# Performance work log

Measured on AMD Instinct MI355X. Metric: run time of the kernel, lower is better.

The kernel has to match this reference:

```python
import jax, jax.numpy as jnp
import numpy as np

N, E = 20000, 320000
DIMS = [(200, 64), (64, 128), (128, 256), (256, 256), (256, 512)]


def _embed(v):
    # NeRF positional encoding, multires=10, include_input, log-sampled freqs, [sin, cos] per freq
    freqs = 2.0 ** jnp.arange(10, dtype=jnp.float32)
    ang = v[:, None, :] * freqs[None, :, None]           # [N, 10, 3]
    sc = jnp.stack([jnp.sin(ang), jnp.cos(ang)], 2)      # [N, 10, 2, 3] (freq-major, sin then cos)
    return jnp.concatenate([v, sc.reshape(v.shape[0], -1)], -1)  # [N, 63]


def _edge_conv(h, src, dst, w1, b1, w2, b2):
    # PyG EdgeConv: nn([x_i, x_j - x_i]) aggregated by mean onto target i
    hi = h[dst]
    hj = h[src]
    m = jnp.concatenate([hi, hj - hi], -1)               # [E, 2*in]
    m = jax.nn.relu(m @ w1 + b1) @ w2 + b2               # [E, out]
    s = jax.ops.segment_sum(m, dst, num_segments=N)
    cnt = jax.ops.segment_sum(jnp.ones((m.shape[0], 1), m.dtype), dst, num_segments=N)
    return s / jnp.maximum(cnt, 1.0)                     # scatter-mean (0 for isolated nodes)


def _bn(h, g, b):
    # training-mode BatchNorm1d over nodes (biased variance, eps=1e-5)
    mu = h.mean(0)
    var = ((h - mu) ** 2).mean(0)
    return g * (h - mu) * jax.lax.rsqrt(var + 1e-5) + b


def setup_inputs() -> dict:
    key = jax.random.key(0)
    keys = iter(jax.random.split(key, 64))
    inp = {
        "x": jax.random.normal(next(keys), (N, 20), jnp.float32),
        "edge_index": jax.random.randint(next(keys), (2, E), 0, N, jnp.int32),
        "batch": jnp.zeros((N,), jnp.int32),
    }
    for i, (din, dout) in enumerate(DIMS, 1):
        inp[f"gc{i}_w1"] = jax.random.normal(next(keys), (2 * din, dout), jnp.float32) / np.sqrt(2.0 * din)
        inp[f"gc{i}_b1"] = jnp.zeros((dout,), jnp.float32)
        inp[f"gc{i}_w2"] = jax.random.normal(next(keys), (dout, dout), jnp.float32) / np.sqrt(1.0 * dout)
        inp[f"gc{i}_b2"] = jnp.zeros((dout,), jnp.float32)
    for i, d in enumerate([64, 128, 256, 256], 1):
        inp[f"n{i}_g"] = jnp.ones((d,), jnp.float32)
        inp[f"n{i}_b"] = jnp.zeros((d,), jnp.float32)
    return inp


def reference(x, edge_index, batch,
              gc1_w1, gc1_b1, gc1_w2, gc1_b2,
              gc2_w1, gc2_b1, gc2_w2, gc2_b2,
              gc3_w1, gc3_b1, gc3_w2, gc3_b2,
              gc4_w1, gc4_b1, gc4_w2, gc4_b2,
              gc5_w1, gc5_b1, gc5_w2, gc5_b2,
              n1_g, n1_b, n2_g, n2_b, n3_g, n3_b, n4_g, n4_b):
    src, dst = edge_index[0], edge_index[1]
    h = jnp.concatenate(
        [_embed(x[:, 0:3]), _embed(x[:, 3:6]), _embed(x[:, 6:9]), x[:, 9:20]], -1)  # [N, 200]
    h = jax.nn.relu(_bn(_edge_conv(h, src, dst, gc1_w1, gc1_b1, gc1_w2, gc1_b2), n1_g, n1_b))
    h = jax.nn.relu(_bn(_edge_conv(h, src, dst, gc2_w1, gc2_b1, gc2_w2, gc2_b2), n2_g, n2_b))
    h = jax.nn.relu(_bn(_edge_conv(h, src, dst, gc3_w1, gc3_b1, gc3_w2, gc3_b2), n3_g, n3_b))
    h = jax.nn.relu(_bn(_edge_conv(h, src, dst, gc4_w1, gc4_b1, gc4_w2, gc4_b2), n4_g, n4_b))
    return _edge_conv(h, src, dst, gc5_w1, gc5_b1, gc5_w2, gc5_b2)  # [N, 512]
```

## Files before the change

kernel.cpp:

```cpp
#include <hip/hip_runtime.h>
#include <math.h>

#define NNODES 20000
#define NEDGES 320000
#define NB 79
#define MBLK 157
#define MQ 19
#define MR 5

typedef __bf16 bf16x8 __attribute__((ext_vector_type(8)));
typedef float f32x4 __attribute__((ext_vector_type(4)));
typedef unsigned short u16x8 __attribute__((ext_vector_type(8)));

__device__ inline unsigned short f2bf(float x) {
  union { float f; unsigned int u; } q;
  q.f = x;
  unsigned int u = q.u;
  unsigned int r = (u + 0x7fffu + ((u >> 16) & 1u)) >> 16;
  return (unsigned short)r;
}

__device__ inline float bf2f(unsigned short u) {
  union { unsigned int u; float f; } q;
  q.u = ((unsigned int)u) << 16;
  return q.f;
}

__device__ inline void load_lds16(const unsigned short* g, unsigned short* l) {
  __builtin_amdgcn_global_load_lds(
      (const __attribute__((address_space(1))) unsigned int*)g,
      (__attribute__((address_space(3))) unsigned int*)l, 16, 0, 0);
}

__global__ __launch_bounds__(256) void init_kernel(int* __restrict__ cnt,
                                                   float* __restrict__ stats) {
  int idx = blockIdx.x * 256 + threadIdx.x;
  if (idx < NNODES) cnt[idx] = 0;
  int j = idx - NNODES;
  if (j >= 0 && j < 4096) stats[j] = 0.f;
}

__global__ __launch_bounds__(256) void count_embed_kernel(
    const int* __restrict__ edst, int* __restrict__ cnt,
    const float* __restrict__ x, unsigned short* __restrict__ h) {
  int bid = blockIdx.x;
  if (bid < 1250) {
    int e = bid * 256 + threadIdx.x;
    atomicAdd(&cnt[edst[e]], 1);
    return;
  }
  int n = (bid - 1250) * 256 + threadIdx.x;
  if (n >= NNODES) return;
  const float* xr = x + (size_t)n * 20;
  unsigned short* hr = h + (size_t)n * 256;
#pragma unroll
  for (int g = 0; g < 3; ++g) {
    float v0 = xr[g * 3 + 0], v1 = xr[g * 3 + 1], v2 = xr[g * 3 + 2];
    unsigned short* o = hr + g * 63;
    o[0] = f2bf(v0); o[1] = f2bf(v1); o[2] = f2bf(v2);
    float f = 1.0f;
    for (int fr = 0; fr < 10; ++fr) {
      float s0, c0, s1, c1, s2, c2;
      sincosf(v0 * f, &s0, &c0);
      sincosf(v1 * f, &s1, &c1);
      sincosf(v2 * f, &s2, &c2);
      int base = 3 + fr * 6;
      o[base + 0] = f2bf(s0); o[base + 1] = f2bf(s1); o[base + 2] = f2bf(s2);
      o[base + 3] = f2bf(c0); o[base + 4] = f2bf(c1); o[base + 5] = f2bf(c2);
      f *= 2.0f;
    }
  }
  for (int j = 0; j < 11; ++j) hr[189 + j] = f2bf(xr[9 + j]);
  for (int j = 200; j < 256; ++j) hr[j] = 0;
}

__global__ __launch_bounds__(256) void scan_pass1(const int* __restrict__ cnt,
                                                  int* __restrict__ bsum) {
  __shared__ int red[256];
  int i = blockIdx.x * 256 + threadIdx.x;
  int v = (i < NNODES) ? cnt[i] : 0;
  red[threadIdx.x] = v;
  __syncthreads();
#pragma unroll
  for (int off = 128; off > 0; off >>= 1) {
    if (threadIdx.x < off) red[threadIdx.x] += red[threadIdx.x + off];
    __syncthreads();
  }
  if (threadIdx.x == 0) bsum[blockIdx.x] = red[0];
}

__global__ __launch_bounds__(128) void scan_pass2(const int* __restrict__ bsum,
                                                  int* __restrict__ boff) {
  __shared__ int buf[128];
  int t = threadIdx.x;
  int v = (t < NB) ? bsum[t] : 0;
  buf[t] = v;
  __syncthreads();
#pragma unroll
  for (int off = 1; off < 128; off <<= 1) {
    int u = (t >= off) ? buf[t - off] : 0;
    __syncthreads();
    buf[t] += u;
    __syncthreads();
  }
  if (t < NB) boff[t] = buf[t] - v;
}

__global__ __launch_bounds__(256) void scan_pass3(const int* __restrict__ cnt,
                                                  const int* __restrict__ boff,
                                                  int* __restrict__ rowptr,
                                                  int* __restrict__ head) {
  __shared__ int buf[256];
  int i = blockIdx.x * 256 + threadIdx.x;
  int v = (i < NNODES) ? cnt[i] : 0;
  buf[threadIdx.x] = v;
  __syncthreads();
#pragma unroll
  for (int off = 1; off < 256; off <<= 1) {
    int u = (threadIdx.x >= off) ? buf[threadIdx.x - off] : 0;
    __syncthreads();
    buf[threadIdx.x] += u;
    __syncthreads();
  }
  if (i < NNODES) {
    int excl = boff[blockIdx.x] + buf[threadIdx.x] - v;
    rowptr[i] = excl;
    head[i] = excl;
  }
  if (i == 0) rowptr[NNODES] = NEDGES;
}

struct WPtrs {
  const float* w1[5];
  const float* w2[5];
};

#define WT1_TOTAL 507904
#define WT2_TOTAL 413696

__global__ __launch_bounds__(256) void scatter_prep_kernel(
    const int* __restrict__ esrc, const int* __restrict__ edst,
    int* __restrict__ head, int* __restrict__ csr_src, WPtrs p,
    unsigned short* __restrict__ Wt1All, unsigned short* __restrict__ Wt2All) {
  int bid = blockIdx.x;
  if (bid < 1250) {
    int e = bid * 256 + threadIdx.x;
    int pos = atomicAdd(&head[edst[e]], 1);
    csr_src[pos] = esrc[e];
    return;
  }
  int idx = (bid - 1250) * 256 + threadIdx.x;
  if (idx < WT1_TOTAL) {
    int L, off, din, dout, Kpad;
    if (idx < 32768)       { L = 0; off = 0;      din = 200; dout = 64;  Kpad = 256; }
    else if (idx < 49152)  { L = 1; off = 32768;  din = 64;  dout = 128; Kpad = 64;  }
    else if (idx < 114688) { L = 2; off = 49152;  din = 128; dout = 256; Kpad = 128; }
    else if (idx < 245760) { L = 3; off = 114688; din = 256; dout = 256; Kpad = 256; }
    else                   { L = 4; off = 245760; din = 256; dout = 512; Kpad = 256; }
    int local = idx - off;
    int c = local / Kpad, k = local % Kpad;
    float v = 0.f;
    if (k < din)
      v = (c < dout) ? p.w1[L][(size_t)k * dout + c]
                     : p.w1[L][(size_t)(din + k) * dout + (c - dout)];
    Wt1All[idx] = f2bf(v);
    return;
  }
  int jdx = idx - WT1_TOTAL;
  if (jdx >= WT2_TOTAL) return;
  int L, off, d;
  if (jdx < 4096)        { L = 0; off = 0;      d = 64;  }
  else if (jdx < 20480)  { L = 1; off = 4096;   d = 128; }
  else if (jdx < 86016)  { L = 2; off = 20480;  d = 256; }
  else if (jdx < 151552) { L = 3; off = 86016;  d = 256; }
  else                   { L = 4; off = 151552; d = 512; }
  int local = jdx - off;
  int n = local / d, k = local % d;
  Wt2All[jdx] = f2bf(p.w2[L][(size_t)k * d + n]);
}

template <int EPI, int EPIA>
__global__ __launch_bounds__(256) void gemm128_kernel(
    const void* __restrict__ Aptr, int lda, int K, int ncolb,
    const unsigned short* __restrict__ Bt, int Ncol, int dhalf,
    const float* __restrict__ bias, const int* __restrict__ cnt,
    const float* __restrict__ pstats, const float* __restrict__ pg,
    const float* __restrict__ pb, float* __restrict__ stats,
    void* __restrict__ Cout) {
  int bid = blockIdx.x;
  int xcd = bid & 7;
  int j = bid >> 3;
  int cntx = MQ + (xcd < MR ? 1 : 0);
  int row_local = j / ncolb;
  if (row_local >= cntx) return;
  int colb = j - row_local * ncolb;
  int row0 = xcd * MQ + min(xcd, MR);
  int bR = (row0 + row_local) * 128;
  int bC = colb * 128;

  __shared__ unsigned short sA[128 * 64];
  __shared__ unsigned short sB[128 * 64];
  __shared__ float sScale[256], sShift[256];
  int tid = threadIdx.x;
  int wid = tid >> 6, lane = tid & 63;
  int wr = wid >> 1, wc = wid & 1;
  int lr = lane & 15, lg = lane >> 4;
  int sub = lane >> 3;
  int ckl = (lane & 7) ^ sub;

  if (EPIA == 1) {
    for (int c = tid; c < K; c += 256) {
      float mu = pstats[c] * (1.0f / NNODES);
      float var = pstats[K + c] * (1.0f / NNODES) - mu * mu;
      float sc = pg[c] * rsqrtf(var + 1e-5f);
      sScale[c] = sc;
      sShift[c] = pb[c] - mu * sc;
    }
    __syncthreads();
  }

  f32x4 acc[4][4];
#pragma unroll
  for (int fr = 0; fr < 4; ++fr)
#pragma unroll
    for (int fc = 0; fc < 4; ++fc) acc[fr][fc] = f32x4{0.f, 0.f, 0.f, 0.f};

  for (int k0 = 0; k0 < K; k0 += 64) {
    if (EPIA == 0) {
      const unsigned short* Ab = (const unsigned short*)Aptr;
#pragma unroll
      for (int q = 0; q < 4; ++q) {
        int t = wid * 4 + q;
        int gr = bR + t * 8 + sub;
        if (gr > NNODES - 1) gr = NNODES - 1;
        load_lds16(Ab + (size_t)gr * lda + k0 + ckl * 8, sA + t * 512);
      }
    } else {
      const float* Af = (const float*)Aptr;
#pragma unroll
      for (int i = 0; i < 4; ++i) {
        int idx = tid + i * 256;
        int row = idx >> 3, c = idx & 7;
        int gr = bR + row;
        u16x8 o;
        if (gr < NNODES) {
          float4 u0 = *(const float4*)(Af + (size_t)gr * lda + k0 + c * 8);
          float4 u1 = *(const float4*)(Af + (size_t)gr * lda + k0 + c * 8 + 4);
          float uv[8] = {u0.x, u0.y, u0.z, u0.w, u1.x, u1.y, u1.z, u1.w};
#pragma unroll
          for (int jj = 0; jj < 8; ++jj) {
            int k = k0 + c * 8 + jj;
            o[jj] = f2bf(fmaxf(uv[jj] * sScale[k] + sShift[k], 0.f));
          }
        } else {
#pragma unroll
          for (int jj = 0; jj < 8; ++jj) o[jj] = 0;
        }
        int ck = c ^ (row & 7);
        *(u16x8*)(sA + row * 64 + ck * 8) = o;
      }
    }
#pragma unroll
    for (int q = 0; q < 4; ++q) {
      int t = wid * 4 + q;
      int gn = bC + t * 8 + sub;
      load_lds16(Bt + (size_t)gn * K + k0 + ckl * 8, sB + t * 512);
    }
    __syncthreads();
#pragma unroll
    for (int ks = 0; ks < 2; ++ks) {
      bf16x8 aF[4], bF[4];
      int cb = ks * 4 + lg;
      int ck = cb ^ (lr & 7);
#pragma unroll
      for (int fr = 0; fr < 4; ++fr)
        aF[fr] = *(const bf16x8*)(sA + (wr * 64 + fr * 16 + lr) * 64 + ck * 8);
#pragma unroll
      for (int fc = 0; fc < 4; ++fc)
        bF[fc] = *(const bf16x8*)(sB + (wc * 64 + fc * 16 + lr) * 64 + ck * 8);
#pragma unroll
      for (int fr = 0; fr < 4; ++fr)
#pragma unroll
        for (int fc = 0; fc < 4; ++fc)
          acc[fr][fc] = __builtin_amdgcn_mfma_f32_16x16x32_bf16(
              aF[fr], bF[fc], acc[fr][fc], 0, 0, 0);
    }
    __syncthreads();
  }

  float csum[4] = {0.f, 0.f, 0.f, 0.f}, csum2[4] = {0.f, 0.f, 0.f, 0.f};
#pragma unroll
  for (int fr = 0; fr < 4; ++fr) {
#pragma unroll
    for (int jj = 0; jj < 4; ++jj) {
      int gr = bR + wr * 64 + fr * 16 + lg * 4 + jj;
      if (gr >= NNODES) continue;
      int ct = (EPI >= 1) ? cnt[gr] : 1;
#pragma unroll
      for (int fc = 0; fc < 4; ++fc) {
        int gc = bC + wc * 64 + fc * 16 + lr;
        float v = acc[fr][fc][jj];
        if (EPI == 0) {
          if (gc < dhalf) v += bias[gc];
          ((unsigned short*)Cout)[(size_t)gr * Ncol + gc] = f2bf(v);
        } else {
          v = (ct > 0) ? (v + bias[gc]) : 0.f;
          ((float*)Cout)[(size_t)gr * Ncol + gc] = v;
          if (EPI == 2) {
            csum[fc] += v;
            csum2[fc] += v * v;
          }
        }
      }
    }
  }
  if (EPI == 2) {
#pragma unroll
    for (int fc = 0; fc < 4; ++fc) {
      float s = csum[fc], s2 = csum2[fc];
      s += __shfl_xor(s, 16, 64);
      s += __shfl_xor(s, 32, 64);
      s2 += __shfl_xor(s2, 16, 64);
      s2 += __shfl_xor(s2, 32, 64);
      if (lg == 0) {
        int gc = bC + wc * 64 + fc * 16 + lr;
        atomicAdd(&stats[gc], s);
        atomicAdd(&stats[Ncol + gc], s2);
      }
    }
  }
}

__global__ __launch_bounds__(256) void gemm64_stats_kernel(
    const unsigned short* __restrict__ A, int lda, int K,
    const unsigned short* __restrict__ Bt, int Ncol,
    const float* __restrict__ bias, const int* __restrict__ cnt,
    float* __restrict__ stats, float* __restrict__ Cout) {
  __shared__ unsigned short sA[128 * 40];
  __shared__ unsigned short sB[64 * 40];
  int tid = threadIdx.x;
  int bR = blockIdx.y * 128, bC = blockIdx.x * 64;
  int wid = tid >> 6, lane = tid & 63;
  int wr = wid >> 1, wc = wid & 1;
  int lr = lane & 15, lg = lane >> 4;

  f32x4 acc[4][2];
#pragma unroll
  for (int fr = 0; fr < 4; ++fr)
#pragma unroll
    for (int fc = 0; fc < 2; ++fc) acc[fr][fc] = f32x4{0.f, 0.f, 0.f, 0.f};

  for (int k0 = 0; k0 < K; k0 += 32) {
#pragma unroll
    for (int rep = 0; rep < 2; ++rep) {
      int idx = tid + rep * 256;
      int row = idx >> 2, kq = (idx & 3) * 8;
      int gr = bR + row;
      bf16x8 v;
      if (gr < NNODES) {
        v = *(const bf16x8*)(A + (size_t)gr * lda + k0 + kq);
      } else {
#pragma unroll
        for (int i = 0; i < 8; ++i) v[i] = (__bf16)0.f;
      }
      *(bf16x8*)(sA + row * 40 + kq) = v;
    }
    {
      int n = tid >> 2, kq = (tid & 3) * 8;
      bf16x8 v = *(const bf16x8*)(Bt + (size_t)(bC + n) * K + k0 + kq);
      *(bf16x8*)(sB + n * 40 + kq) = v;
    }
    __syncthreads();
    bf16x8 aF[4], bF[2];
#pragma unroll
    for (int fr = 0; fr < 4; ++fr)
      aF[fr] = *(const bf16x8*)(sA + (wr * 64 + fr * 16 + lr) * 40 + lg * 8);
#pragma unroll
    for (int fc = 0; fc < 2; ++fc)
      bF[fc] = *(const bf16x8*)(sB + (wc * 32 + fc * 16 + lr) * 40 + lg * 8);
#pragma unroll
    for (int fr = 0; fr < 4; ++fr)
#pragma unroll
      for (int fc = 0; fc < 2; ++fc)
        acc[fr][fc] = __builtin_amdgcn_mfma_f32_16x16x32_bf16(
            aF[fr], bF[fc], acc[fr][fc], 0, 0, 0);
    __syncthreads();
  }

  float csum[2] = {0.f, 0.f}, csum2[2] = {0.f, 0.f};
#pragma unroll
  for (int fr = 0; fr < 4; ++fr) {
#pragma unroll
    for (int j = 0; j < 4; ++j) {
      int gr = bR + wr * 64 + fr * 16 + lg * 4 + j;
      if (gr >= NNODES) continue;
      int ct = cnt[gr];
#pragma unroll
      for (int fc = 0; fc < 2; ++fc) {
        int gc = bC + wc * 32 + fc * 16 + lr;
        float v = acc[fr][fc][j];
        v = (ct > 0) ? (v + bias[gc]) : 0.f;
        Cout[(size_t)gr * Ncol + gc] = v;
        csum[fc] += v;
        csum2[fc] += v * v;
      }
    }
  }
#pragma unroll
  for (int fc = 0; fc < 2; ++fc) {
    float s = csum[fc], s2 = csum2[fc];
    s += __shfl_xor(s, 16, 64);
    s += __shfl_xor(s, 32, 64);
    s2 += __shfl_xor(s2, 16, 64);
    s2 += __shfl_xor(s2, 32, 64);
    if (lg == 0) {
      int gc = bC + wc * 32 + fc * 16 + lr;
      atomicAdd(&stats[gc], s);
      atomicAdd(&stats[Ncol + gc], s2);
    }
  }
}

template <int D, int SLICES>
__global__ __launch_bounds__(256) void edge_agg_kernel(
    const unsigned short* __restrict__ AV, const int* __restrict__ rowptr,
    const int* __restrict__ csr_src, unsigned short* __restrict__ Y) {
  int slice = blockIdx.x % SLICES;
  int ngrp = blockIdx.x / SLICES;
  int tid = threadIdx.x;
  int ln = tid & 7;
  int sn = tid >> 3;
  int node = ngrp * 32 + sn;
  if (node >= NNODES) return;
  int c = slice * 64 + ln * 8;
  const unsigned short* Arow = AV + (size_t)node * 2 * D;
  u16x8 a8 = *(const u16x8*)(Arow + c);
  u16x8 v8 = *(const u16x8*)(Arow + D + c);
  float ad[8], acc[8];
#pragma unroll
  for (int i = 0; i < 8; ++i) {
    ad[i] = bf2f(a8[i]) - bf2f(v8[i]);
    acc[i] = 0.f;
  }
  int e0 = rowptr[node], e1 = rowptr[node + 1];
  int e = e0;
  for (; e + 3 < e1; e += 4) {
    int s0 = csr_src[e], s1 = csr_src[e + 1];
    int s2 = csr_src[e + 2], s3 = csr_src[e + 3];
    u16x8 w0 = *(const u16x8*)(AV + (size_t)s0 * 2 * D + D + c);
    u16x8 w1 = *(const u16x8*)(AV + (size_t)s1 * 2 * D + D + c);
    u16x8 w2 = *(const u16x8*)(AV + (size_t)s2 * 2 * D + D + c);
    u16x8 w3 = *(const u16x8*)(AV + (size_t)s3 * 2 * D + D + c);
#pragma unroll
    for (int i = 0; i < 8; ++i) {
      acc[i] += fmaxf(ad[i] + bf2f(w0[i]), 0.f) + fmaxf(ad[i] + bf2f(w1[i]), 0.f) +
                fmaxf(ad[i] + bf2f(w2[i]), 0.f) + fmaxf(ad[i] + bf2f(w3[i]), 0.f);
    }
  }
  for (; e < e1; ++e) {
    int s0 = csr_src[e];
    u16x8 w0 = *(const u16x8*)(AV + (size_t)s0 * 2 * D + D + c);
#pragma unroll
    for (int i = 0; i < 8; ++i) acc[i] += fmaxf(ad[i] + bf2f(w0[i]), 0.f);
  }
  float inv = (e1 > e0) ? 1.f / (float)(e1 - e0) : 0.f;
  u16x8 o;
#pragma unroll
  for (int i = 0; i < 8; ++i) o[i] = f2bf(acc[i] * inv);
  *(u16x8*)(Y + (size_t)node * D + c) = o;
}

static void launch_edge_agg(int dout, const unsigned short* AV, const int* rowptr,
                            const int* csr_src, unsigned short* Y,
                            hipStream_t st) {
  const int NG = (NNODES + 31) / 32;
  switch (dout) {
    case 64:
      hipLaunchKernelGGL((edge_agg_kernel<64, 1>), dim3(NG * 1), dim3(256), 0, st,
                         AV, rowptr, csr_src, Y);
      break;
    case 128:
      hipLaunchKernelGGL((edge_agg_kernel<128, 2>), dim3(NG * 2), dim3(256), 0, st,
                         AV, rowptr, csr_src, Y);
      break;
    case 256:
      hipLaunchKernelGGL((edge_agg_kernel<256, 4>), dim3(NG * 4), dim3(256), 0, st,
                         AV, rowptr, csr_src, Y);
      break;
    case 512:
      hipLaunchKernelGGL((edge_agg_kernel<512, 8>), dim3(NG * 8), dim3(256), 0, st,
                         AV, rowptr, csr_src, Y);
      break;
  }
}

extern "C" void kernel_launch(void* const* d_in, const int* in_sizes, int n_in,
                              void* d_out, int out_size, void* d_ws,
                              size_t ws_size, hipStream_t stream) {
  const float* x = (const float*)d_in[0];
  const int* edge_index = (const int*)d_in[1];
  const int* esrc = edge_index;
  const int* edst = edge_index + NEDGES;

  const float* gw1[5] = {(const float*)d_in[3],  (const float*)d_in[7],
                         (const float*)d_in[11], (const float*)d_in[15],
                         (const float*)d_in[19]};
  const float* gb1[5] = {(const float*)d_in[4],  (const float*)d_in[8],
                         (const float*)d_in[12], (const float*)d_in[16],
                         (const float*)d_in[20]};
  const float* gw2[5] = {(const float*)d_in[5],  (const float*)d_in[9],
                         (const float*)d_in[13], (const float*)d_in[17],
                         (const float*)d_in[21]};
  const float* gb2[5] = {(const float*)d_in[6],  (const float*)d_in[10],
                         (const float*)d_in[14], (const float*)d_in[18],
                         (const float*)d_in[22]};
  const float* ng[4] = {(const float*)d_in[23], (const float*)d_in[25],
                        (const float*)d_in[27], (const float*)d_in[29]};
  const float* nb[4] = {(const float*)d_in[24], (const float*)d_in[26],
                        (const float*)d_in[28], (const float*)d_in[30]};

  unsigned short* AV = (unsigned short*)d_ws;
  float* S = (float*)(AV + (size_t)NNODES * 1024);
  unsigned short* Hbf = (unsigned short*)(S + (size_t)NNODES * 256);
  unsigned short* Ybf = Hbf + (size_t)NNODES * 256;
  unsigned short* Wt1All = Ybf + (size_t)NNODES * 512;
  unsigned short* Wt2All = Wt1All + WT1_TOTAL;
  int* cnt = (int*)(Wt2All + WT2_TOTAL);
  int* rowptr = cnt + NNODES;
  int* head = rowptr + NNODES + 1;
  int* csr_src = head + NNODES;
  int* bsum = csr_src + NEDGES;
  int* boff = bsum + NB;
  float* stats = (float*)(boff + NB);

  const int Kpads[5] = {256, 64, 128, 256, 256};
  const int douts[5] = {64, 128, 256, 256, 512};
  const int wt1_off[5] = {0, 32768, 49152, 114688, 245760};
  const int wt2_off[5] = {0, 4096, 20480, 86016, 151552};

  WPtrs wp;
  for (int i = 0; i < 5; ++i) { wp.w1[i] = gw1[i]; wp.w2[i] = gw2[i]; }

  init_kernel<<<(NNODES + 4096 + 255) / 256, 256, 0, stream>>>(cnt, stats);
  count_embed_kernel<<<1250 + NB, 256, 0, stream>>>(edst, cnt, x, Hbf);
  scan_pass1<<<NB, 256, 0, stream>>>(cnt, bsum);
  scan_pass2<<<1, 128, 0, stream>>>(bsum, boff);
  scan_pass3<<<NB, 256, 0, stream>>>(cnt, boff, rowptr, head);
  scatter_prep_kernel<<<1250 + (WT1_TOTAL + WT2_TOTAL + 255) / 256, 256, 0, stream>>>(
      esrc, edst, head, csr_src, wp, Wt1All, Wt2All);

  int lda = 256;
  for (int L = 0; L < 5; ++L) {
    int Kp = Kpads[L], dout = douts[L];
    {
      int ncolb = 2 * dout / 128;
      if (ncolb < 1) ncolb = 1;
      dim3 g1(8 * (MQ + 1) * ncolb);
      if (L == 0) {
        hipLaunchKernelGGL((gemm128_kernel<0, 0>), g1, dim3(256), 0, stream,
                           (const void*)Hbf, lda, Kp, ncolb, Wt1All + wt1_off[L],
                           2 * dout, dout, gb1[L], (const int*)nullptr,
                           (const float*)nullptr, (const float*)nullptr,
                           (const float*)nullptr, (float*)nullptr, (void*)AV);
      } else {
        hipLaunchKernelGGL((gemm128_kernel<0, 1>), g1, dim3(256), 0, stream,
                           (const void*)S, Kp, Kp, ncolb, Wt1All + wt1_off[L],
                           2 * dout, dout, gb1[L], (const int*)nullptr,
                           stats + (L - 1) * 1024, ng[L - 1], nb[L - 1],
                           (float*)nullptr, (void*)AV);
      }
    }
    launch_edge_agg(dout, AV, rowptr, csr_src, Ybf, stream);
    if (L == 0) {
      dim3 g2(1, MBLK);
      gemm64_stats_kernel<<<g2, 256, 0, stream>>>(
          Ybf, dout, dout, Wt2All + wt2_off[L], dout, gb2[L], cnt,
          stats + L * 1024, S);
    } else if (L < 4) {
      int ncolb = dout / 128;
      dim3 g2(8 * (MQ + 1) * ncolb);
      hipLaunchKernelGGL((gemm128_kernel<2, 0>), g2, dim3(256), 0, stream,
                         (const void*)Ybf, dout, dout, ncolb, Wt2All + wt2_off[L],
                         dout, dout, gb2[L], cnt, (const float*)nullptr,
                         (const float*)nullptr, (const float*)nullptr,
                         stats + L * 1024, (void*)S);
    } else {
      int ncolb = dout / 128;
      dim3 g2(8 * (MQ + 1) * ncolb);
      hipLaunchKernelGGL((gemm128_kernel<1, 0>), g2, dim3(256), 0, stream,
                         (const void*)Ybf, dout, dout, ncolb, Wt2All + wt2_off[L],
                         dout, dout, gb2[L], cnt, (const float*)nullptr,
                         (const float*)nullptr, (const float*)nullptr,
                         (float*)nullptr, (void*)d_out);
    }
  }
}
```

Measured before the change: 448.1 us.

## Double-buffer LDS tiles in node GEMM to overlap global loads with MFMA

Turns the node-level GEMM's K loop into a two-stage pipeline: A and B tiles for the next K step are fetched into a second LDS buffer while MFMAs run on the current one, with one barrier per iteration instead of two. For the BN-fused input path, the fp32 prefetch goes into registers and the BN+ReLU+bf16 conversion is written to the next buffer after the MFMAs. BN scale/shift is now computed per thread from stats rather than through a shared-memory table. This doubles LDS use, which may reduce occupancy, and adds register pressure from the prefetched floats.

After: 482.0 us. +7.6%, slower.

```diff
diff --git a/kernel.cpp b/kernel.cpp
--- a/kernel.cpp
+++ b/kernel.cpp
@@ -177,6 +177,44 @@
   int local = jdx - off;
   int n = local / d, k = local % d;
   Wt2All[jdx] = f2bf(p.w2[L][(size_t)k * d + n]);
+}
+
+__device__ inline void bn_convert_store(const float4* pre, const float* pstats,
+                                        const float* pg, const float* pb, int K,
+                                        int kb, int tid, unsigned short* dst) {
+  float4 m0 = *(const float4*)(pstats + kb);
+  float4 m1 = *(const float4*)(pstats + kb + 4);
+  float4 q0 = *(const float4*)(pstats + K + kb);
+  float4 q1 = *(const float4*)(pstats + K + kb + 4);
+  float4 g0 = *(const float4*)(pg + kb);
+  float4 g1 = *(const float4*)(pg + kb + 4);
+  float4 b0 = *(const float4*)(pb + kb);
+  float4 b1 = *(const float4*)(pb + kb + 4);
+  float mu8[8] = {m0.x, m0.y, m0.z, m0.w, m1.x, m1.y, m1.z, m1.w};
+  float q8[8] = {q0.x, q0.y, q0.z, q0.w, q1.x, q1.y, q1.z, q1.w};
+  float g8[8] = {g0.x, g0.y, g0.z, g0.w, g1.x, g1.y, g1.z, g1.w};
+  float b8[8] = {b0.x, b0.y, b0.z, b0.w, b1.x, b1.y, b1.z, b1.w};
+  float sc[8], sh[8];
+#pragma unroll
+  for (int j = 0; j < 8; ++j) {
+    float mu = mu8[j] * (1.0f / NNODES);
+    float var = q8[j] * (1.0f / NNODES) - mu * mu;
+    float s = g8[j] * rsqrtf(var + 1e-5f);
+    sc[j] = s;
+    sh[j] = b8[j] - mu * s;
+  }
+#pragma unroll
+  for (int i = 0; i < 4; ++i) {
+    int idx = tid + i * 256;
+    int row = idx >> 3;
+    int ck = (tid & 7) ^ (row & 7);
+    const float* u = (const float*)&pre[i * 2];
+    u16x8 o;
+#pragma unroll
+    for (int j = 0; j < 8; ++j)
+      o[j] = f2bf(fmaxf(u[j] * sc[j] + sh[j], 0.f));
+    *(u16x8*)(dst + row * 64 + ck * 8) = o;
+  }
 }
 
 template <int EPI, int EPIA>
@@ -198,9 +236,8 @@
   int bR = (row0 + row_local) * 128;
   int bC = colb * 128;
 
-  __shared__ unsigned short sA[128 * 64];
-  __shared__ unsigned short sB[128 * 64];
-  __shared__ float sScale[256], sShift[256];
+  __shared__ unsigned short sA0[128 * 64], sA1[128 * 64];
+  __shared__ unsigned short sB0[128 * 64], sB1[128 * 64];
   int tid = threadIdx.x;
   int wid = tid >> 6, lane = tid & 63;
   int wr = wid >> 1, wc = wid & 1;
@@ -208,65 +245,91 @@
   int sub = lane >> 3;
   int ckl = (lane & 7) ^ sub;
 
-  if (EPIA == 1) {
-    for (int c = tid; c < K; c += 256) {
-      float mu = pstats[c] * (1.0f / NNODES);
-      float var = pstats[K + c] * (1.0f / NNODES) - mu * mu;
-      float sc = pg[c] * rsqrtf(var + 1e-5f);
-      sScale[c] = sc;
-      sShift[c] = pb[c] - mu * sc;
-    }
-    __syncthreads();
-  }
-
   f32x4 acc[4][4];
 #pragma unroll
   for (int fr = 0; fr < 4; ++fr)
 #pragma unroll
     for (int fc = 0; fc < 4; ++fc) acc[fr][fc] = f32x4{0.f, 0.f, 0.f, 0.f};
 
-  for (int k0 = 0; k0 < K; k0 += 64) {
-    if (EPIA == 0) {
-      const unsigned short* Ab = (const unsigned short*)Aptr;
+  unsigned short* cA = sA0;
+  unsigned short* cB = sB0;
+  unsigned short* nA = sA1;
+  unsigned short* nB = sB1;
+  const int nt = K >> 6;
+
+  if (EPIA == 0) {
+    const unsigned short* Ab = (const unsigned short*)Aptr;
+#pragma unroll
+    for (int q = 0; q < 4; ++q) {
+      int tt = wid * 4 + q;
+      int gr = bR + tt * 8 + sub;
+      if (gr > NNODES - 1) gr = NNODES - 1;
+      load_lds16(Ab + (size_t)gr * lda + ckl * 8, cA + tt * 512);
+    }
+  } else {
+    const float* Af = (const float*)Aptr;
+    float4 pre[8];
+#pragma unroll
+    for (int i = 0; i < 4; ++i) {
+      int idx = tid + i * 256;
+      int gr = bR + (idx >> 3);
+      if (gr < NNODES) {
+        pre[i * 2] = *(const float4*)(Af + (size_t)gr * lda + (tid & 7) * 8);
+        pre[i * 2 + 1] = *(const float4*)(Af + (size_t)gr * lda + (tid & 7) * 8 + 4);
+      } else {
+        pre[i * 2] = float4{0.f, 0.f, 0.f, 0.f};
+        pre[i * 2 + 1] = float4{0.f, 0.f, 0.f, 0.f};
+      }
+    }
+    bn_convert_store(pre, pstats, pg, pb, K, (tid & 7) * 8, tid, cA);
+  }
+#pragma unroll
+  for (int q = 0; q < 4; ++q) {
+    int tt = wid * 4 + q;
+    int gn = bC + tt * 8 + sub;
+    load_lds16(Bt + (size_t)gn * K + ckl * 8, cB + tt * 512);
+  }
+  __syncthreads();
+
+  for (int t = 0; t < nt; ++t) {
+    __builtin_amdgcn_sched_barrier(0);
+    const bool pf = (t + 1 < nt);
+    const int k1 = (t + 1) << 6;
+    float4 pre[8];
+    if (pf) {
+      if (EPIA == 0) {
+        const unsigned short* Ab = (const unsigned short*)Aptr;
+#pragma unroll
+        for (int q = 0; q < 4; ++q) {
+          int tt = wid * 4 + q;
+          int gr = bR + tt * 8 + sub;
+          if (gr > NNODES - 1) gr = NNODES - 1;
+          load_lds16(Ab + (size_t)gr * lda + k1 + ckl * 8, nA + tt * 512);
+        }
+      } else {
+        const float* Af = (const float*)Aptr;
+#pragma unroll
+        for (int i = 0; i < 4; ++i) {
+          int idx = tid + i * 256;
+          int gr = bR + (idx >> 3);
+          if (gr < NNODES) {
+            pre[i * 2] = *(const float4*)(Af + (size_t)gr * lda + k1 + (tid & 7) * 8);
+            pre[i * 2 + 1] =
+                *(const float4*)(Af + (size_t)gr * lda + k1 + (tid & 7) * 8 + 4);
+          } else {
+            pre[i * 2] = float4{0.f, 0.f, 0.f, 0.f};
+            pre[i * 2 + 1] = float4{0.f, 0.f, 0.f, 0.f};
+          }
+        }
+      }
 #pragma unroll
       for (int q = 0; q < 4; ++q) {
-        int t = wid * 4 + q;
-        int gr = bR + t * 8 + sub;
-        if (gr > NNODES - 1) gr = NNODES - 1;
-        load_lds16(Ab + (size_t)gr * lda + k0 + ckl * 8, sA + t * 512);
-      }
-    } else {
-      const float* Af = (const float*)Aptr;
-#pragma unroll
-      for (int i = 0; i < 4; ++i) {
-        int idx = tid + i * 256;
-        int row = idx >> 3, c = idx & 7;
-        int gr = bR + row;
-        u16x8 o;
-        if (gr < NNODES) {
-          float4 u0 = *(const float4*)(Af + (size_t)gr * lda + k0 + c * 8);
-          float4 u1 = *(const float4*)(Af + (size_t)gr * lda + k0 + c * 8 + 4);
-          float uv[8] = {u0.x, u0.y, u0.z, u0.w, u1.x, u1.y, u1.z, u1.w};
-#pragma unroll
-          for (int jj = 0; jj < 8; ++jj) {
-            int k = k0 + c * 8 + jj;
-            o[jj] = f2bf(fmaxf(uv[jj] * sScale[k] + sShift[k], 0.f));
-          }
-        } else {
-#pragma unroll
-          for (int jj = 0; jj < 8; ++jj) o[jj] = 0;
-        }
-        int ck = c ^ (row & 7);
-        *(u16x8*)(sA + row * 64 + ck * 8) = o;
-      }
-    }
-#pragma unroll
-    for (int q = 0; q < 4; ++q) {
-      int t = wid * 4 + q;
-      int gn = bC + t * 8 + sub;
-      load_lds16(Bt + (size_t)gn * K + k0 + ckl * 8, sB + t * 512);
-    }
-    __syncthreads();
+        int tt = wid * 4 + q;
+        int gn = bC + tt * 8 + sub;
+        load_lds16(Bt + (size_t)gn * K + k1 + ckl * 8, nB + tt * 512);
+      }
+    }
+    __builtin_amdgcn_sched_barrier(0);
 #pragma unroll
     for (int ks = 0; ks < 2; ++ks) {
       bf16x8 aF[4], bF[4];
@@ -274,10 +337,10 @@
       int ck = cb ^ (lr & 7);
 #pragma unroll
       for (int fr = 0; fr < 4; ++fr)
-        aF[fr] = *(const bf16x8*)(sA + (wr * 64 + fr * 16 + lr) * 64 + ck * 8);
+        aF[fr] = *(const bf16x8*)(cA + (wr * 64 + fr * 16 + lr) * 64 + ck * 8);
 #pragma unroll
       for (int fc = 0; fc < 4; ++fc)
-        bF[fc] = *(const bf16x8*)(sB + (wc * 64 + fc * 16 + lr) * 64 + ck * 8);
+        bF[fc] = *(const bf16x8*)(cB + (wc * 64 + fc * 16 + lr) * 64 + ck * 8);
 #pragma unroll
       for (int fr = 0; fr < 4; ++fr)
 #pragma unroll
@@ -285,7 +348,14 @@
           acc[fr][fc] = __builtin_amdgcn_mfma_f32_16x16x32_bf16(
               aF[fr], bF[fc], acc[fr][fc], 0, 0, 0);
     }
-    __syncthreads();
+    __builtin_amdgcn_sched_barrier(0);
+    if (EPIA == 1 && pf)
+      bn_convert_store(pre, pstats, pg, pb, K, k1 + (tid & 7) * 8, tid, nA);
+    asm volatile("s_waitcnt vmcnt(0) lgkmcnt(0)" ::: "memory");
+    __builtin_amdgcn_s_barrier();
+    unsigned short* tp;
+    tp = cA; cA = nA; nA = tp;
+    tp = cB; cB = nB; nB = tp;
   }
 
   float csum[4] = {0.f, 0.f, 0.f, 0.f}, csum2[4] = {0.f, 0.f, 0.f, 0.f};
```

## Store pre-BatchNorm layer outputs in bf16 and fold block-offset scan into pass3

Applied to the files above, without the earlier changes.

The second GEMM's output S, which is the pre-BatchNorm activation, is now written as bf16 instead of fp32. The next layer's A-load reads it as bf16 and applies the BN scale, shift and ReLU after converting back, which halves the store and reload traffic for that intermediate. Statistics are still accumulated in fp32 before rounding. Separately, the single-block scan_pass2 launch is removed and every pass3 block recomputes the 79-entry prefix itself, trading redundant work for one fewer launch. The bf16 rounding of the pre-BN values adds some precision loss.

Result: no change. 447.7 us (-0.1%).

```diff
diff --git a/kernel.cpp b/kernel.cpp
--- a/kernel.cpp
+++ b/kernel.cpp
@@ -89,41 +89,39 @@
   if (threadIdx.x == 0) bsum[blockIdx.x] = red[0];
 }
 
-__global__ __launch_bounds__(128) void scan_pass2(const int* __restrict__ bsum,
-                                                  int* __restrict__ boff) {
-  __shared__ int buf[128];
+__global__ __launch_bounds__(256) void scan_pass3(const int* __restrict__ cnt,
+                                                  const int* __restrict__ bsum,
+                                                  int* __restrict__ rowptr,
+                                                  int* __restrict__ head) {
+  __shared__ int pref[128];
+  __shared__ int buf[256];
   int t = threadIdx.x;
-  int v = (t < NB) ? bsum[t] : 0;
+  if (t < 128) {
+    int v = (t < NB) ? bsum[t] : 0;
+    pref[t] = v;
+  }
+  __syncthreads();
+#pragma unroll
+  for (int off = 1; off < 128; off <<= 1) {
+    int u = (t < 128 && t >= off) ? pref[t - off] : 0;
+    __syncthreads();
+    if (t < 128) pref[t] += u;
+    __syncthreads();
+  }
+  int boff = (blockIdx.x == 0) ? 0 : pref[blockIdx.x - 1];
+  int i = blockIdx.x * 256 + t;
+  int v = (i < NNODES) ? cnt[i] : 0;
   buf[t] = v;
   __syncthreads();
 #pragma unroll
-  for (int off = 1; off < 128; off <<= 1) {
+  for (int off = 1; off < 256; off <<= 1) {
     int u = (t >= off) ? buf[t - off] : 0;
     __syncthreads();
     buf[t] += u;
     __syncthreads();
   }
-  if (t < NB) boff[t] = buf[t] - v;
-}
-
-__global__ __launch_bounds__(256) void scan_pass3(const int* __restrict__ cnt,
-                                                  const int* __restrict__ boff,
-                                                  int* __restrict__ rowptr,
-                                                  int* __restrict__ head) {
-  __shared__ int buf[256];
-  int i = blockIdx.x * 256 + threadIdx.x;
-  int v = (i < NNODES) ? cnt[i] : 0;
-  buf[threadIdx.x] = v;
-  __syncthreads();
-#pragma unroll
-  for (int off = 1; off < 256; off <<= 1) {
-    int u = (threadIdx.x >= off) ? buf[threadIdx.x - off] : 0;
-    __syncthreads();
-    buf[threadIdx.x] += u;
-    __syncthreads();
-  }
   if (i < NNODES) {
-    int excl = boff[blockIdx.x] + buf[threadIdx.x] - v;
+    int excl = boff + buf[t] - v;
     rowptr[i] = excl;
     head[i] = excl;
   }
@@ -236,7 +234,7 @@
         load_lds16(Ab + (size_t)gr * lda + k0 + ckl * 8, sA + t * 512);
       }
     } else {
-      const float* Af = (const float*)Aptr;
+      const unsigned short* Ab = (const unsigned short*)Aptr;
 #pragma unroll
       for (int i = 0; i < 4; ++i) {
         int idx = tid + i * 256;
@@ -244,13 +242,11 @@
         int gr = bR + row;
         u16x8 o;
         if (gr < NNODES) {
-          float4 u0 = *(const float4*)(Af + (size_t)gr * lda + k0 + c * 8);
-          float4 u1 = *(const float4*)(Af + (size_t)gr * lda + k0 + c * 8 + 4);
-          float uv[8] = {u0.x, u0.y, u0.z, u0.w, u1.x, u1.y, u1.z, u1.w};
+          u16x8 s8 = *(const u16x8*)(Ab + (size_t)gr * lda + k0 + c * 8);
 #pragma unroll
           for (int jj = 0; jj < 8; ++jj) {
             int k = k0 + c * 8 + jj;
-            o[jj] = f2bf(fmaxf(uv[jj] * sScale[k] + sShift[k], 0.f));
+            o[jj] = f2bf(fmaxf(bf2f(s8[jj]) * sScale[k] + sShift[k], 0.f));
           }
         } else {
 #pragma unroll
@@ -303,13 +299,14 @@
         if (EPI == 0) {
           if (gc < dhalf) v += bias[gc];
           ((unsigned short*)Cout)[(size_t)gr * Ncol + gc] = f2bf(v);
+        } else if (EPI == 1) {
+          v = (ct > 0) ? (v + bias[gc]) : 0.f;
+          ((float*)Cout)[(size_t)gr * Ncol + gc] = v;
         } else {
           v = (ct > 0) ? (v + bias[gc]) : 0.f;
-          ((float*)Cout)[(size_t)gr * Ncol + gc] = v;
-          if (EPI == 2) {
-            csum[fc] += v;
-            csum2[fc] += v * v;
-          }
+          ((unsigned short*)Cout)[(size_t)gr * Ncol + gc] = f2bf(v);
+          csum[fc] += v;
+          csum2[fc] += v * v;
         }
       }
     }
@@ -335,7 +332,7 @@
     const unsigned short* __restrict__ A, int lda, int K,
     const unsigned short* __restrict__ Bt, int Ncol,
     const float* __restrict__ bias, const int* __restrict__ cnt,
-    float* __restrict__ stats, float* __restrict__ Cout) {
+    float* __restrict__ stats, unsigned short* __restrict__ Cout) {
   __shared__ unsigned short sA[128 * 40];
   __shared__ unsigned short sB[64 * 40];
   int tid = threadIdx.x;
@@ -400,7 +397,7 @@
         int gc = bC + wc * 32 + fc * 16 + lr;
         float v = acc[fr][fc][j];
         v = (ct > 0) ? (v + bias[gc]) : 0.f;
-        Cout[(size_t)gr * Ncol + gc] = v;
+        Cout[(size_t)gr * Ncol + gc] = f2bf(v);
         csum[fc] += v;
         csum2[fc] += v * v;
       }
@@ -520,8 +517,8 @@
                         (const float*)d_in[28], (const float*)d_in[30]};
 
   unsigned short* AV = (unsigned short*)d_ws;
-  float* S = (float*)(AV + (size_t)NNODES * 1024);
-  unsigned short* Hbf = (unsigned short*)(S + (size_t)NNODES * 256);
+  unsigned short* S = AV + (size_t)NNODES * 1024;
+  unsigned short* Hbf = S + (size_t)NNODES * 256;
   unsigned short* Ybf = Hbf + (size_t)NNODES * 256;
   unsigned short* Wt1All = Ybf + (size_t)NNODES * 512;
   unsigned short* Wt2All = Wt1All + WT1_TOTAL;
@@ -530,8 +527,7 @@
   int* head = rowptr + NNODES + 1;
   int* csr_src = head + NNODES;
   int* bsum = csr_src + NEDGES;
-  int* boff = bsum + NB;
-  float* stats = (float*)(boff + NB);
+  float* stats = (float*)(bsum + NB + 1);
 
   const int Kpads[5] = {256, 64, 128, 256, 256};
   const int douts[5] = {64, 128, 256, 256, 512};
@@ -544,8 +540,7 @@
   init_kernel<<<(NNODES + 4096 + 255) / 256, 256, 0, stream>>>(cnt, stats);
   count_embed_kernel<<<1250 + NB, 256, 0, stream>>>(edst, cnt, x, Hbf);
   scan_pass1<<<NB, 256, 0, stream>>>(cnt, bsum);
-  scan_pass2<<<1, 128, 0, stream>>>(bsum, boff);
-  scan_pass3<<<NB, 256, 0, stream>>>(cnt, boff, rowptr, head);
+  scan_pass3<<<NB, 256, 0, stream>>>(cnt, bsum, rowptr, head);
   scatter_prep_kernel<<<1250 + (WT1_TOTAL + WT2_TOTAL + 255) / 256, 256, 0, stream>>>(
       esrc, edst, head, csr_src, wp, Wt1All, Wt2All);
 
```
